# Performance work log

Hardware: AMD Instinct MI355X
Metric: run time of the kernel (lower is better)

Reference implementation:

```python
import jax, jax.numpy as jnp
import numpy as np

NUM_EMBEDDINGS = 1024
EMBEDDING_DIM = 128
COMMITMENT_COST = 0.25


def setup_inputs() -> dict:
    key = jax.random.key(0)
    k_in, k_cb = jax.random.split(key)
    inputs = jax.random.normal(k_in, (65536, EMBEDDING_DIM), dtype=jnp.float32)
    # torch init: uniform(-1/K, 1/K)
    codebook = jax.random.uniform(
        k_cb, (NUM_EMBEDDINGS, EMBEDDING_DIM), dtype=jnp.float32,
        minval=-1.0 / NUM_EMBEDDINGS, maxval=1.0 / NUM_EMBEDDINGS)
    return {"inputs": inputs, "codebook": codebook}


def reference(inputs, codebook):
    # inputs: [N, D], codebook: [K, D]
    # squared euclidean distances [N, K]
    distances = (jnp.sum(inputs ** 2, axis=1, keepdims=True)
                 + jnp.sum(codebook ** 2, axis=1)
                 - 2.0 * jnp.matmul(inputs, codebook.T))
    encoding_indices = jnp.argmin(distances, axis=1)  # [N]
    encodings = jax.nn.one_hot(encoding_indices, NUM_EMBEDDINGS, dtype=jnp.float32)  # [N, K]
    # onehot @ codebook == gather
    quantized = jnp.take(codebook, encoding_indices, axis=0)  # [N, D]

    e_latent_loss = jnp.mean((jax.lax.stop_gradient(quantized) - inputs) ** 2)
    q_latent_loss = jnp.mean((quantized - jax.lax.stop_gradient(inputs)) ** 2)
    loss = q_latent_loss + COMMITMENT_COST * e_latent_loss

    # straight-through estimator
    quantized_st = inputs + jax.lax.stop_gradient(quantized - inputs)

    avg_probs = jnp.mean(encodings, axis=0)  # [K]
    perplexity = jnp.exp(-jnp.sum(avg_probs * jnp.log(avg_probs + 1e-10)))
    return (loss, quantized_st, perplexity, encodings)
```

## Files before the change

kernel.cpp:

```cpp
#include <hip/hip_runtime.h>

#define NROWS 65536
#define DIM   128
#define KC    1024
#define QST_OFF  1
#define PPL_OFF  8388609
#define ENC_OFF  8388610

typedef float floatx4 __attribute__((ext_vector_type(4)));
typedef _Float16 half8_t __attribute__((ext_vector_type(8)));
typedef _Float16 half4_t __attribute__((ext_vector_type(4)));

#define BSTR 144
#define CIMG 4608
#define CCH  9216
#define A_LO 9216
#define RPB 64

__device__ __forceinline__ float fadd_rn_(float a, float b) {
#pragma clang fp contract(off)
  return a + b;
}
__device__ __forceinline__ float fsub_rn_(float a, float b) {
#pragma clang fp contract(off)
  return a - b;
}
__device__ __forceinline__ float fmul_rn_(float a, float b) {
#pragma clang fp contract(off)
  return a * b;
}

__device__ __forceinline__ void async_ld16(const void* g, void* l) {
  __builtin_amdgcn_global_load_lds(
      (const __attribute__((address_space(1))) void*)g,
      (__attribute__((address_space(3))) void*)l, 16, 0, 0);
}

__device__ __forceinline__ float rowsq128(const float4* src) {
  float r[8];
  {
    float4 v0 = src[0], v1 = src[1];
    r[0] = fmul_rn_(v0.x, v0.x); r[1] = fmul_rn_(v0.y, v0.y);
    r[2] = fmul_rn_(v0.z, v0.z); r[3] = fmul_rn_(v0.w, v0.w);
    r[4] = fmul_rn_(v1.x, v1.x); r[5] = fmul_rn_(v1.y, v1.y);
    r[6] = fmul_rn_(v1.z, v1.z); r[7] = fmul_rn_(v1.w, v1.w);
  }
  for (int i = 1; i < 16; ++i) {
    float4 v0 = src[2 * i], v1 = src[2 * i + 1];
    r[0] = fadd_rn_(r[0], fmul_rn_(v0.x, v0.x));
    r[1] = fadd_rn_(r[1], fmul_rn_(v0.y, v0.y));
    r[2] = fadd_rn_(r[2], fmul_rn_(v0.z, v0.z));
    r[3] = fadd_rn_(r[3], fmul_rn_(v0.w, v0.w));
    r[4] = fadd_rn_(r[4], fmul_rn_(v1.x, v1.x));
    r[5] = fadd_rn_(r[5], fmul_rn_(v1.y, v1.y));
    r[6] = fadd_rn_(r[6], fmul_rn_(v1.z, v1.z));
    r[7] = fadd_rn_(r[7], fmul_rn_(v1.w, v1.w));
  }
  return fadd_rn_(fadd_rn_(fadd_rn_(r[0], r[1]), fadd_rn_(r[2], r[3])),
                  fadd_rn_(fadd_rn_(r[4], r[5]), fadd_rn_(r[6], r[7])));
}

__global__ __launch_bounds__(256) void k_prep(const float* __restrict__ cb,
                                              float* __restrict__ cbT,
                                              float* __restrict__ cc,
                                              _Float16* __restrict__ Bp) {
  __shared__ float tile[64 * 129];
  int t = threadIdx.x;
  int c0 = blockIdx.x * 64;
#pragma unroll
  for (int it = 0; it < 32; ++it) {
    int f = it * 256 + t;
    int c = f >> 7, d = f & 127;
    tile[c * 129 + d] = cb[(size_t)(c0 + c) * DIM + d];
  }
  __syncthreads();
#pragma unroll
  for (int it = 0; it < 32; ++it) {
    int f = it * 256 + t;
    int d = f >> 6, c = f & 63;
    cbT[(size_t)d * KC + c0 + c] = tile[c * 129 + d];
  }
  if (t < 64) {
    const float* s = &tile[t * 129];
    float r[8];
#pragma unroll
    for (int j = 0; j < 8; ++j) r[j] = fmul_rn_(s[j], s[j]);
    for (int i = 1; i < 16; ++i) {
#pragma unroll
      for (int j = 0; j < 8; ++j)
        r[j] = fadd_rn_(r[j], fmul_rn_(s[i * 8 + j], s[i * 8 + j]));
    }
    float ccv = fadd_rn_(fadd_rn_(fadd_rn_(r[0], r[1]), fadd_rn_(r[2], r[3])),
                         fadd_rn_(fadd_rn_(r[4], r[5]), fadd_rn_(r[6], r[7])));
    cc[c0 + t] = ccv;
    int g = c0 + t;
    size_t base = (size_t)(g >> 5) * CCH + (size_t)(g & 31) * BSTR;
#pragma unroll
    for (int k = 128; k < 144; ++k) {
      Bp[base + k] = (_Float16)0.0f;
      Bp[base + CIMG + k] = (_Float16)0.0f;
    }
    Bp[base + 128] = (_Float16)(-512.0f * ccv);
  }
#pragma unroll
  for (int it = 0; it < 32; ++it) {
    int f = it * 256 + t;
    int c = f >> 7, k = f & 127;
    int g = c0 + c;
    size_t base = (size_t)(g >> 5) * CCH + (size_t)(g & 31) * BSTR;
    float c5 = tile[c * 129 + k] * 512.0f;
    _Float16 h = (_Float16)c5;
    _Float16 l = (_Float16)(c5 - (float)h);
    Bp[base + k] = h;
    Bp[base + CIMG + k] = l;
  }
}

__global__ __launch_bounds__(256, 4) void k_main(const float* __restrict__ inp,
                                                 const float* __restrict__ cb,
                                                 const float* __restrict__ cbT,
                                                 const _Float16* __restrict__ Bp,
                                                 const float* __restrict__ cc,
                                                 float* __restrict__ out_qst,
                                                 float* __restrict__ out_enc,
                                                 int* __restrict__ cnt,
                                                 float* __restrict__ lsum) {
  __shared__ _Float16 SB[2 * CCH];
  __shared__ float xxs[RPB];
  __shared__ int bk[RPB];
  __shared__ int fl_rows[RPB];
  __shared__ int fl_cnt;
  __shared__ float xs[128];
  __shared__ float redd[4];
  __shared__ int redi[4];
  __shared__ float redf[4];

  int t = threadIdx.x;
  int lane = t & 63, w = t >> 6;
  int q = lane >> 4, col = lane & 15;
  int row0 = blockIdx.x * RPB;
  if (t == 0) fl_cnt = 0;

  {
    int r = t & 63, seg = t >> 6;
    const float* src = inp + (size_t)(row0 + r) * DIM + seg * 32;
#pragma unroll
    for (int i = 0; i < 8; ++i) {
      float4 v = *(const float4*)(src + i * 4);
      _Float16 h0 = (_Float16)v.x, h1 = (_Float16)v.y, h2 = (_Float16)v.z, h3 = (_Float16)v.w;
      half4_t hv = {h0, h1, h2, h3};
      half4_t lv = {(_Float16)(v.x - (float)h0), (_Float16)(v.y - (float)h1),
                    (_Float16)(v.z - (float)h2), (_Float16)(v.w - (float)h3)};
      int k = seg * 32 + i * 4;
      *(half4_t*)&SB[r * BSTR + k] = hv;
      *(half4_t*)&SB[A_LO + r * BSTR + k] = lv;
    }
  }
  if (t < RPB) xxs[t] = rowsq128((const float4*)(inp + (size_t)(row0 + t) * DIM));
  __syncthreads();

  int arow = w * 16 + col;
  half8_t ah[4], al[4];
#pragma unroll
  for (int ks = 0; ks < 4; ++ks) {
    ah[ks] = *(const half8_t*)&SB[arow * BSTR + ks * 32 + q * 8];
    al[ks] = *(const half8_t*)&SB[A_LO + arow * BSTR + ks * 32 + q * 8];
  }
  float xr[4];
#pragma unroll
  for (int r = 0; r < 4; ++r) xr[r] = xxs[w * 16 + q * 4 + r];
  __syncthreads();

  half8_t aex = {0, 0, 0, 0, 0, 0, 0, 0};
  if (q == 0) aex[0] = (_Float16)0.5f;

  float b1[4], b2[4];
  int i1[4];
#pragma unroll
  for (int r = 0; r < 4; ++r) { b1[r] = -3.4e38f; b2[r] = -3.4e38f; i1[r] = 0; }

  const float4* bp4 = (const float4*)Bp;
  floatx4* enc4 = (floatx4*)(out_enc + (size_t)row0 * KC);

  {
    const float4* gsrc = bp4;
#pragma unroll
    for (int r = 0; r < 4; ++r)
      async_ld16(gsrc + r * 256 + t, &SB[(size_t)(r * 256 + t) * 8]);
    if (t < 128) async_ld16(gsrc + 1024 + t, &SB[(size_t)(1024 + t) * 8]);
  }
  asm volatile("s_waitcnt vmcnt(0)" ::: "memory");
  __builtin_amdgcn_sched_barrier(0);
  __builtin_amdgcn_s_barrier();
  __builtin_amdgcn_sched_barrier(0);

  for (int c = 0; c < 32; ++c) {
    if (c > 0) {
      asm volatile("s_waitcnt vmcnt(2)" ::: "memory");
      __builtin_amdgcn_sched_barrier(0);
      __builtin_amdgcn_s_barrier();
      __builtin_amdgcn_sched_barrier(0);
    }
    if (c < 31) {
      const float4* gsrc = bp4 + (size_t)(c + 1) * 1152;
      int boff = ((c + 1) & 1) * CCH;
#pragma unroll
      for (int r = 0; r < 4; ++r)
        async_ld16(gsrc + r * 256 + t, &SB[boff + (size_t)(r * 256 + t) * 8]);
      if (t < 128) async_ld16(gsrc + 1024 + t, &SB[boff + (size_t)(1024 + t) * 8]);
    }
    __builtin_amdgcn_sched_barrier(0);
    {
      floatx4 z = {0.f, 0.f, 0.f, 0.f};
      __builtin_nontemporal_store(z, enc4 + (size_t)c * 512 + t);
      __builtin_nontemporal_store(z, enc4 + (size_t)c * 512 + 256 + t);
    }
    __builtin_amdgcn_sched_barrier(0);

    const _Float16* Bb = &SB[(c & 1) * CCH];
    floatx4 acc[2];
    acc[0] = (floatx4){0.f, 0.f, 0.f, 0.f};
    acc[1] = (floatx4){0.f, 0.f, 0.f, 0.f};

#pragma unroll
    for (int ks = 0; ks < 4; ++ks) {
#pragma unroll
      for (int ct = 0; ct < 2; ++ct) {
        int brow = ct * 16 + col;
        half8_t bh = *(const half8_t*)&Bb[brow * BSTR + ks * 32 + q * 8];
        half8_t bl = *(const half8_t*)&Bb[CIMG + brow * BSTR + ks * 32 + q * 8];
        acc[ct] = __builtin_amdgcn_mfma_f32_16x16x32_f16(ah[ks], bh, acc[ct], 0, 0, 0);
        acc[ct] = __builtin_amdgcn_mfma_f32_16x16x32_f16(ah[ks], bl, acc[ct], 0, 0, 0);
        acc[ct] = __builtin_amdgcn_mfma_f32_16x16x32_f16(al[ks], bh, acc[ct], 0, 0, 0);
      }
    }
#pragma unroll
    for (int ct = 0; ct < 2; ++ct) {
      int brow = ct * 16 + col;
      half8_t bex = *(const half8_t*)&Bb[brow * BSTR + 128];
      acc[ct] = __builtin_amdgcn_mfma_f32_16x16x32_f16(aex, bex, acc[ct], 0, 0, 0);
    }

#pragma unroll
    for (int ct = 0; ct < 2; ++ct) {
      int kidx = c * 32 + ct * 16 + col;
#pragma unroll
      for (int r = 0; r < 4; ++r) {
        float s = acc[ct][r];
        bool gt = s > b1[r];
        b2[r] = gt ? b1[r] : fmaxf(b2[r], s);
        i1[r] = gt ? kidx : i1[r];
        b1[r] = gt ? s : b1[r];
      }
    }
  }

#pragma unroll
  for (int r = 0; r < 4; ++r) {
    float v1 = b1[r], v2 = b2[r];
    int ii = i1[r];
    for (int off = 1; off < 16; off <<= 1) {
      float ov1 = __shfl_xor(v1, off);
      float ov2 = __shfl_xor(v2, off);
      int oi = __shfl_xor(ii, off);
      float nb1 = fmaxf(v1, ov1);
      float nb2 = fmaxf(fminf(v1, ov1), fmaxf(v2, ov2));
      ii = (ov1 > v1) ? oi : ((ov1 < v1) ? ii : min(ii, oi));
      v1 = nb1; v2 = nb2;
    }
    b1[r] = v1; b2[r] = v2; i1[r] = ii;
  }

  if (col == 0) {
#pragma unroll
    for (int r = 0; r < 4; ++r) {
      int lrow = w * 16 + q * 4 + r;
      bk[lrow] = i1[r];
      float dist1 = fsub_rn_(xr[r], fmul_rn_(b1[r], 0.00390625f));
      float u = (dist1 >= 256.f) ? 9.4e-5f : 4.7e-5f;
      if (b1[r] - b2[r] < u * 256.0f) {
        int p = atomicAdd(&fl_cnt, 1);
        fl_rows[p] = lrow;
      }
    }
  }
  __syncthreads();

  int nf = fl_cnt;
  for (int f = 0; f < nf; ++f) {
    int row = fl_rows[f];
    if (t < 128) xs[t] = inp[(size_t)(row0 + row) * DIM + t];
    __syncthreads();
    float xxr = xxs[row];
    int c0 = t * 4;
    float a0 = 0.f, a1 = 0.f, a2 = 0.f, a3 = 0.f;
    for (int d = 0; d < 128; ++d) {
      float xd = xs[d];
      float4 cv = *(const float4*)&cbT[(size_t)d * KC + c0];
      a0 = __builtin_fmaf(xd, cv.x, a0);
      a1 = __builtin_fmaf(xd, cv.y, a1);
      a2 = __builtin_fmaf(xd, cv.z, a2);
      a3 = __builtin_fmaf(xd, cv.w, a3);
    }
    float aa[4] = {a0, a1, a2, a3};
    float bb = 3.4e38f;
    int bi = 0;
#pragma unroll
    for (int j = 0; j < 4; ++j) {
      float dist = fsub_rn_(fadd_rn_(xxr, cc[c0 + j]), fmul_rn_(2.0f, aa[j]));
      if (dist < bb) { bb = dist; bi = c0 + j; }
    }
    for (int off = 1; off < 64; off <<= 1) {
      float ov = __shfl_xor(bb, off);
      int oi = __shfl_xor(bi, off);
      if (ov < bb || (ov == bb && oi < bi)) { bb = ov; bi = oi; }
    }
    if (lane == 0) { redd[w] = bb; redi[w] = bi; }
    __syncthreads();
    if (t == 0) {
      float vb = redd[0];
      int ib = redi[0];
#pragma unroll
      for (int ww = 1; ww < 4; ++ww) {
        if (redd[ww] < vb || (redd[ww] == vb && redi[ww] < ib)) { vb = redd[ww]; ib = redi[ww]; }
      }
      bk[row] = ib;
    }
    __syncthreads();
  }

  if (t < RPB) atomicAdd(&cnt[bk[t]], 1);

  float ls = 0.f;
#pragma unroll 4
  for (int it = 0; it < 32; ++it) {
    int f = it * 256 + t;
    int row = f >> 7, d = f & 127;
    size_t gro = (size_t)(row0 + row) * DIM + d;
    float x = inp[gro];
    float qv = cb[(size_t)bk[row] * DIM + d];
    float qe = fsub_rn_(qv, x);
    __builtin_nontemporal_store(fadd_rn_(x, qe), &out_qst[gro]);
    ls = __builtin_fmaf(qe, qe, ls);
  }

  if (t < RPB) out_enc[(size_t)(row0 + t) * KC + bk[t]] = 1.0f;

  for (int off = 32; off; off >>= 1) ls += __shfl_down(ls, off);
  if (lane == 0) redf[w] = ls;
  __syncthreads();
  if (t == 0) atomicAdd(lsum, redf[0] + redf[1] + redf[2] + redf[3]);
}

__global__ __launch_bounds__(1024) void k_scalars(const int* __restrict__ cnt,
                                                  const float* __restrict__ lsum,
                                                  float* __restrict__ out) {
  int t = threadIdx.x;
  float p = (float)cnt[t] * (1.0f / 65536.0f);
  float term = fmul_rn_(p, logf(fadd_rn_(p, 1e-10f)));
  for (int off = 32; off; off >>= 1) term += __shfl_down(term, off);
  __shared__ float red[16];
  if ((t & 63) == 0) red[t >> 6] = term;
  __syncthreads();
  if (t == 0) {
    float s = 0.f;
#pragma unroll
    for (int w = 0; w < 16; ++w) s += red[w];
    out[PPL_OFF] = expf(-s);
    float e = *lsum * (1.0f / 8388608.0f);
    out[0] = fadd_rn_(e, fmul_rn_(0.25f, e));
  }
}

extern "C" void kernel_launch(void* const* d_in, const int* in_sizes, int n_in,
                              void* d_out, int out_size, void* d_ws, size_t ws_size,
                              hipStream_t stream) {
  const float* inp = (const float*)d_in[0];
  const float* cb = (const float*)d_in[1];
  float* out = (float*)d_out;

  _Float16* Bp = (_Float16*)d_ws;
  float* cbT = (float*)(Bp + 32 * CCH);
  float* cc = cbT + DIM * KC;
  int* cnt = (int*)(cc + KC);
  float* lsum = (float*)(cnt + KC);

  (void)hipMemsetAsync(cnt, 0, (KC + 1) * sizeof(int), stream);
  k_prep<<<KC / 64, 256, 0, stream>>>(cb, cbT, cc, Bp);
  k_main<<<NROWS / RPB, 256, 0, stream>>>(inp, cb, cbT, Bp, cc,
                                          out + QST_OFF, out + ENC_OFF, cnt, lsum);
  k_scalars<<<1, 1024, 0, stream>>>(cnt, lsum, out);
}
```

Measured before the change: 391.8 us.

## Read codebook B fragments directly from global memory instead of LDS double-buffering

```diff
diff --git a/kernel.cpp b/kernel.cpp
--- a/kernel.cpp
+++ b/kernel.cpp
@@ -28,12 +28,6 @@
 __device__ __forceinline__ float fmul_rn_(float a, float b) {
 #pragma clang fp contract(off)
   return a * b;
-}
-
-__device__ __forceinline__ void async_ld16(const void* g, void* l) {
-  __builtin_amdgcn_global_load_lds(
-      (const __attribute__((address_space(1))) void*)g,
-      (__attribute__((address_space(3))) void*)l, 16, 0, 0);
 }
 
 __device__ __forceinline__ float rowsq128(const float4* src) {
@@ -142,18 +136,18 @@
   if (t == 0) fl_cnt = 0;
 
   {
-    int r = t & 63, seg = t >> 6;
-    const float* src = inp + (size_t)(row0 + r) * DIM + seg * 32;
-#pragma unroll
-    for (int i = 0; i < 8; ++i) {
-      float4 v = *(const float4*)(src + i * 4);
+    const float* src = inp + (size_t)row0 * DIM;
+#pragma unroll
+    for (int it = 0; it < 8; ++it) {
+      int f = it * 256 + t;
+      int r = f >> 5, c4 = f & 31;
+      float4 v = *(const float4*)(src + (size_t)r * DIM + c4 * 4);
       _Float16 h0 = (_Float16)v.x, h1 = (_Float16)v.y, h2 = (_Float16)v.z, h3 = (_Float16)v.w;
       half4_t hv = {h0, h1, h2, h3};
       half4_t lv = {(_Float16)(v.x - (float)h0), (_Float16)(v.y - (float)h1),
                     (_Float16)(v.z - (float)h2), (_Float16)(v.w - (float)h3)};
-      int k = seg * 32 + i * 4;
-      *(half4_t*)&SB[r * BSTR + k] = hv;
-      *(half4_t*)&SB[A_LO + r * BSTR + k] = lv;
+      *(half4_t*)&SB[r * BSTR + c4 * 4] = hv;
+      *(half4_t*)&SB[A_LO + r * BSTR + c4 * 4] = lv;
     }
   }
   if (t < RPB) xxs[t] = rowsq128((const float4*)(inp + (size_t)(row0 + t) * DIM));
@@ -169,7 +163,6 @@
   float xr[4];
 #pragma unroll
   for (int r = 0; r < 4; ++r) xr[r] = xxs[w * 16 + q * 4 + r];
-  __syncthreads();
 
   half8_t aex = {0, 0, 0, 0, 0, 0, 0, 0};
   if (q == 0) aex[0] = (_Float16)0.5f;
@@ -179,45 +172,17 @@
 #pragma unroll
   for (int r = 0; r < 4; ++r) { b1[r] = -3.4e38f; b2[r] = -3.4e38f; i1[r] = 0; }
 
-  const float4* bp4 = (const float4*)Bp;
   floatx4* enc4 = (floatx4*)(out_enc + (size_t)row0 * KC);
-
-  {
-    const float4* gsrc = bp4;
-#pragma unroll
-    for (int r = 0; r < 4; ++r)
-      async_ld16(gsrc + r * 256 + t, &SB[(size_t)(r * 256 + t) * 8]);
-    if (t < 128) async_ld16(gsrc + 1024 + t, &SB[(size_t)(1024 + t) * 8]);
-  }
-  asm volatile("s_waitcnt vmcnt(0)" ::: "memory");
-  __builtin_amdgcn_sched_barrier(0);
-  __builtin_amdgcn_s_barrier();
-  __builtin_amdgcn_sched_barrier(0);
+  const _Float16* bbase = Bp + (size_t)col * BSTR + q * 8;
 
   for (int c = 0; c < 32; ++c) {
-    if (c > 0) {
-      asm volatile("s_waitcnt vmcnt(2)" ::: "memory");
-      __builtin_amdgcn_sched_barrier(0);
-      __builtin_amdgcn_s_barrier();
-      __builtin_amdgcn_sched_barrier(0);
-    }
-    if (c < 31) {
-      const float4* gsrc = bp4 + (size_t)(c + 1) * 1152;
-      int boff = ((c + 1) & 1) * CCH;
-#pragma unroll
-      for (int r = 0; r < 4; ++r)
-        async_ld16(gsrc + r * 256 + t, &SB[boff + (size_t)(r * 256 + t) * 8]);
-      if (t < 128) async_ld16(gsrc + 1024 + t, &SB[boff + (size_t)(1024 + t) * 8]);
-    }
-    __builtin_amdgcn_sched_barrier(0);
     {
       floatx4 z = {0.f, 0.f, 0.f, 0.f};
       __builtin_nontemporal_store(z, enc4 + (size_t)c * 512 + t);
       __builtin_nontemporal_store(z, enc4 + (size_t)c * 512 + 256 + t);
     }
-    __builtin_amdgcn_sched_barrier(0);
-
-    const _Float16* Bb = &SB[(c & 1) * CCH];
+
+    const _Float16* Bc = bbase + (size_t)c * CCH;
     floatx4 acc[2];
     acc[0] = (floatx4){0.f, 0.f, 0.f, 0.f};
     acc[1] = (floatx4){0.f, 0.f, 0.f, 0.f};
@@ -226,9 +191,9 @@
     for (int ks = 0; ks < 4; ++ks) {
 #pragma unroll
       for (int ct = 0; ct < 2; ++ct) {
-        int brow = ct * 16 + col;
-        half8_t bh = *(const half8_t*)&Bb[brow * BSTR + ks * 32 + q * 8];
-        half8_t bl = *(const half8_t*)&Bb[CIMG + brow * BSTR + ks * 32 + q * 8];
+        const _Float16* p = Bc + ct * (16 * BSTR) + ks * 32;
+        half8_t bh = *(const half8_t*)p;
+        half8_t bl = *(const half8_t*)(p + CIMG);
         acc[ct] = __builtin_amdgcn_mfma_f32_16x16x32_f16(ah[ks], bh, acc[ct], 0, 0, 0);
         acc[ct] = __builtin_amdgcn_mfma_f32_16x16x32_f16(ah[ks], bl, acc[ct], 0, 0, 0);
         acc[ct] = __builtin_amdgcn_mfma_f32_16x16x32_f16(al[ks], bh, acc[ct], 0, 0, 0);
@@ -236,8 +201,8 @@
     }
 #pragma unroll
     for (int ct = 0; ct < 2; ++ct) {
-      int brow = ct * 16 + col;
-      half8_t bex = *(const half8_t*)&Bb[brow * BSTR + 128];
+      const _Float16* p = Bp + (size_t)c * CCH + (size_t)(ct * 16 + col) * BSTR + 128;
+      half8_t bex = *(const half8_t*)p;
       acc[ct] = __builtin_amdgcn_mfma_f32_16x16x32_f16(aex, bex, acc[ct], 0, 0, 0);
     }
 
```

Result: slower. 479.3 us (+22.3%).

## Split MFMA work by codebook column half per wave, sharing B fragments across two row tiles

Applied to the files above, without the earlier changes.

```diff
diff --git a/kernel.cpp b/kernel.cpp
--- a/kernel.cpp
+++ b/kernel.cpp
@@ -134,50 +134,55 @@
   __shared__ float redd[4];
   __shared__ int redi[4];
   __shared__ float redf[4];
+  __shared__ float mb1[RPB][2];
+  __shared__ float mb2[RPB][2];
+  __shared__ int mi1[RPB][2];
 
   int t = threadIdx.x;
   int lane = t & 63, w = t >> 6;
   int q = lane >> 4, col = lane & 15;
+  int half = w & 1;
+  int wrow = (w >> 1) * 32;
   int row0 = blockIdx.x * RPB;
   if (t == 0) fl_cnt = 0;
 
   {
-    int r = t & 63, seg = t >> 6;
-    const float* src = inp + (size_t)(row0 + r) * DIM + seg * 32;
-#pragma unroll
-    for (int i = 0; i < 8; ++i) {
-      float4 v = *(const float4*)(src + i * 4);
+    const float* src = inp + (size_t)row0 * DIM;
+#pragma unroll
+    for (int it = 0; it < 8; ++it) {
+      int f = it * 256 + t;
+      int r = f >> 5, c4 = f & 31;
+      float4 v = *(const float4*)(src + (size_t)r * DIM + c4 * 4);
       _Float16 h0 = (_Float16)v.x, h1 = (_Float16)v.y, h2 = (_Float16)v.z, h3 = (_Float16)v.w;
       half4_t hv = {h0, h1, h2, h3};
       half4_t lv = {(_Float16)(v.x - (float)h0), (_Float16)(v.y - (float)h1),
                     (_Float16)(v.z - (float)h2), (_Float16)(v.w - (float)h3)};
-      int k = seg * 32 + i * 4;
-      *(half4_t*)&SB[r * BSTR + k] = hv;
-      *(half4_t*)&SB[A_LO + r * BSTR + k] = lv;
+      *(half4_t*)&SB[r * BSTR + c4 * 4] = hv;
+      *(half4_t*)&SB[A_LO + r * BSTR + c4 * 4] = lv;
     }
   }
   if (t < RPB) xxs[t] = rowsq128((const float4*)(inp + (size_t)(row0 + t) * DIM));
   __syncthreads();
 
-  int arow = w * 16 + col;
-  half8_t ah[4], al[4];
+  int arow0 = wrow + col;
+  int arow1 = arow0 + 16;
+  half8_t ah0[4], al0[4], ah1[4], al1[4];
 #pragma unroll
   for (int ks = 0; ks < 4; ++ks) {
-    ah[ks] = *(const half8_t*)&SB[arow * BSTR + ks * 32 + q * 8];
-    al[ks] = *(const half8_t*)&SB[A_LO + arow * BSTR + ks * 32 + q * 8];
-  }
-  float xr[4];
-#pragma unroll
-  for (int r = 0; r < 4; ++r) xr[r] = xxs[w * 16 + q * 4 + r];
+    ah0[ks] = *(const half8_t*)&SB[arow0 * BSTR + ks * 32 + q * 8];
+    al0[ks] = *(const half8_t*)&SB[A_LO + arow0 * BSTR + ks * 32 + q * 8];
+    ah1[ks] = *(const half8_t*)&SB[arow1 * BSTR + ks * 32 + q * 8];
+    al1[ks] = *(const half8_t*)&SB[A_LO + arow1 * BSTR + ks * 32 + q * 8];
+  }
   __syncthreads();
 
   half8_t aex = {0, 0, 0, 0, 0, 0, 0, 0};
   if (q == 0) aex[0] = (_Float16)0.5f;
 
-  float b1[4], b2[4];
-  int i1[4];
-#pragma unroll
-  for (int r = 0; r < 4; ++r) { b1[r] = -3.4e38f; b2[r] = -3.4e38f; i1[r] = 0; }
+  float b1[8], b2[8];
+  int i1[8];
+#pragma unroll
+  for (int j = 0; j < 8; ++j) { b1[j] = -3.4e38f; b2[j] = -3.4e38f; i1[j] = 0; }
 
   const float4* bp4 = (const float4*)Bp;
   floatx4* enc4 = (floatx4*)(out_enc + (size_t)row0 * KC);
@@ -218,47 +223,52 @@
     __builtin_amdgcn_sched_barrier(0);
 
     const _Float16* Bb = &SB[(c & 1) * CCH];
-    floatx4 acc[2];
-    acc[0] = (floatx4){0.f, 0.f, 0.f, 0.f};
-    acc[1] = (floatx4){0.f, 0.f, 0.f, 0.f};
+    floatx4 acc0 = (floatx4){0.f, 0.f, 0.f, 0.f};
+    floatx4 acc1 = (floatx4){0.f, 0.f, 0.f, 0.f};
+    int brow = half * 16 + col;
 
 #pragma unroll
     for (int ks = 0; ks < 4; ++ks) {
-#pragma unroll
-      for (int ct = 0; ct < 2; ++ct) {
-        int brow = ct * 16 + col;
-        half8_t bh = *(const half8_t*)&Bb[brow * BSTR + ks * 32 + q * 8];
-        half8_t bl = *(const half8_t*)&Bb[CIMG + brow * BSTR + ks * 32 + q * 8];
-        acc[ct] = __builtin_amdgcn_mfma_f32_16x16x32_f16(ah[ks], bh, acc[ct], 0, 0, 0);
-        acc[ct] = __builtin_amdgcn_mfma_f32_16x16x32_f16(ah[ks], bl, acc[ct], 0, 0, 0);
-        acc[ct] = __builtin_amdgcn_mfma_f32_16x16x32_f16(al[ks], bh, acc[ct], 0, 0, 0);
-      }
-    }
-#pragma unroll
-    for (int ct = 0; ct < 2; ++ct) {
-      int brow = ct * 16 + col;
+      const _Float16* p = &Bb[brow * BSTR + ks * 32 + q * 8];
+      half8_t bh = *(const half8_t*)p;
+      half8_t bl = *(const half8_t*)(p + CIMG);
+      acc0 = __builtin_amdgcn_mfma_f32_16x16x32_f16(ah0[ks], bh, acc0, 0, 0, 0);
+      acc0 = __builtin_amdgcn_mfma_f32_16x16x32_f16(ah0[ks], bl, acc0, 0, 0, 0);
+      acc0 = __builtin_amdgcn_mfma_f32_16x16x32_f16(al0[ks], bh, acc0, 0, 0, 0);
+      acc1 = __builtin_amdgcn_mfma_f32_16x16x32_f16(ah1[ks], bh, acc1, 0, 0, 0);
+      acc1 = __builtin_amdgcn_mfma_f32_16x16x32_f16(ah1[ks], bl, acc1, 0, 0, 0);
+      acc1 = __builtin_amdgcn_mfma_f32_16x16x32_f16(al1[ks], bh, acc1, 0, 0, 0);
+    }
+    {
       half8_t bex = *(const half8_t*)&Bb[brow * BSTR + 128];
-      acc[ct] = __builtin_amdgcn_mfma_f32_16x16x32_f16(aex, bex, acc[ct], 0, 0, 0);
-    }
-
-#pragma unroll
-    for (int ct = 0; ct < 2; ++ct) {
-      int kidx = c * 32 + ct * 16 + col;
-#pragma unroll
-      for (int r = 0; r < 4; ++r) {
-        float s = acc[ct][r];
+      acc0 = __builtin_amdgcn_mfma_f32_16x16x32_f16(aex, bex, acc0, 0, 0, 0);
+      acc1 = __builtin_amdgcn_mfma_f32_16x16x32_f16(aex, bex, acc1, 0, 0, 0);
+    }
+
+    int kidx = c * 32 + half * 16 + col;
+#pragma unroll
+    for (int r = 0; r < 4; ++r) {
+      {
+        float s = acc0[r];
         bool gt = s > b1[r];
         b2[r] = gt ? b1[r] : fmaxf(b2[r], s);
         i1[r] = gt ? kidx : i1[r];
         b1[r] = gt ? s : b1[r];
       }
-    }
-  }
-
-#pragma unroll
-  for (int r = 0; r < 4; ++r) {
-    float v1 = b1[r], v2 = b2[r];
-    int ii = i1[r];
+      {
+        float s = acc1[r];
+        bool gt = s > b1[4 + r];
+        b2[4 + r] = gt ? b1[4 + r] : fmaxf(b2[4 + r], s);
+        i1[4 + r] = gt ? kidx : i1[4 + r];
+        b1[4 + r] = gt ? s : b1[4 + r];
+      }
+    }
+  }
+
+#pragma unroll
+  for (int j = 0; j < 8; ++j) {
+    float v1 = b1[j], v2 = b2[j];
+    int ii = i1[j];
     for (int off = 1; off < 16; off <<= 1) {
       float ov1 = __shfl_xor(v1, off);
       float ov2 = __shfl_xor(v2, off);
@@ -268,20 +278,38 @@
       ii = (ov1 > v1) ? oi : ((ov1 < v1) ? ii : min(ii, oi));
       v1 = nb1; v2 = nb2;
     }
-    b1[r] = v1; b2[r] = v2; i1[r] = ii;
+    b1[j] = v1; b2[j] = v2; i1[j] = ii;
   }
 
   if (col == 0) {
 #pragma unroll
-    for (int r = 0; r < 4; ++r) {
-      int lrow = w * 16 + q * 4 + r;
-      bk[lrow] = i1[r];
-      float dist1 = fsub_rn_(xr[r], fmul_rn_(b1[r], 0.00390625f));
-      float u = (dist1 >= 256.f) ? 9.4e-5f : 4.7e-5f;
-      if (b1[r] - b2[r] < u * 256.0f) {
-        int p = atomicAdd(&fl_cnt, 1);
-        fl_rows[p] = lrow;
+    for (int s = 0; s < 2; ++s) {
+#pragma unroll
+      for (int r = 0; r < 4; ++r) {
+        int j = s * 4 + r;
+        int row = wrow + s * 16 + q * 4 + r;
+        mb1[row][half] = b1[j];
+        mb2[row][half] = b2[j];
+        mi1[row][half] = i1[j];
       }
+    }
+  }
+  __syncthreads();
+
+  if (t < RPB) {
+    float a1 = mb1[t][0], a2 = mb2[t][0];
+    int ai = mi1[t][0];
+    float c1 = mb1[t][1], c2 = mb2[t][1];
+    int ci = mi1[t][1];
+    float v1 = fmaxf(a1, c1);
+    float v2 = fmaxf(fminf(a1, c1), fmaxf(a2, c2));
+    int ii = (c1 > a1) ? ci : ((c1 < a1) ? ai : min(ai, ci));
+    bk[t] = ii;
+    float dist1 = fsub_rn_(xxs[t], fmul_rn_(v1, 0.00390625f));
+    float u = (dist1 >= 256.f) ? 9.4e-5f : 4.7e-5f;
+    if (v1 - v2 < u * 256.0f) {
+      int p = atomicAdd(&fl_cnt, 1);
+      fl_rows[p] = t;
     }
   }
   __syncthreads();
```

New measurement: 389.8 us. No clear change (-0.5%).
